# Kernel tuning notes

Hardware: AMD Instinct MI355X
Metric: run time of the kernel (lower is better)

The kernel has to match this reference:

```python
import jax, jax.numpy as jnp
import numpy as np

D = 128          # embed_d
T = 10           # MAX_NEIGHBORS
L = 2            # n_layers
B = 4096
ND, FD = 20000, 2048
NG, FG = 20000, 1024
NC, FC = 10000, 512


def setup_inputs() -> dict:
    key = jax.random.key(0)
    ks = jax.random.split(key, 18)
    inp = {
        'drug_feats': jax.random.normal(ks[0], (ND, FD), jnp.float32),
        'gene_feats': jax.random.normal(ks[1], (NG, FG), jnp.float32),
        'cell_feats': jax.random.normal(ks[2], (NC, FC), jnp.float32),
        'Wd': jax.random.normal(ks[3], (FD, D), jnp.float32) / np.sqrt(FD),
        'bd': jnp.zeros((D,), jnp.float32),
        'Wg': jax.random.normal(ks[4], (FG, D), jnp.float32) / np.sqrt(FG),
        'bg': jnp.zeros((D,), jnp.float32),
        'Wc': jax.random.normal(ks[5], (FC, D), jnp.float32) / np.sqrt(FC),
        'bc': jnp.zeros((D,), jnp.float32),
        'gru_W': jax.random.normal(ks[6], (L, 3, D, 3 * D), jnp.float32) / np.sqrt(D),
        'gru_U': jax.random.normal(ks[7], (L, 3, D, 3 * D), jnp.float32) / np.sqrt(D),
        'gru_b': jnp.zeros((L, 3, 3 * D), jnp.float32),
        'att': jax.random.normal(ks[8], (L, 2 * D), jnp.float32) / np.sqrt(2 * D),
        'ids': jax.random.randint(ks[9], (B,), 0, ND, jnp.int32),
        # neighbor ids in [-1, N-1]; -1 == PAD_VALUE
        'neigh_drug': jax.random.randint(ks[10], (B, T), 0, ND + 1, jnp.int32) - 1,
        'neigh_gene': jax.random.randint(ks[11], (B, T), 0, NG + 1, jnp.int32) - 1,
        'neigh_cell': jax.random.randint(ks[12], (B, T), 0, NC + 1, jnp.int32) - 1,
    }
    return inp


def _proj_gather(table, W, b, idx):
    # gather raw features by id (PAD -> zeros) then project, matching
    # conteng_agg + masked scatter in node_het_agg.
    mask = (idx >= 0)                              # [B, T]
    safe = jnp.clip(idx, 0, None)
    f = table[safe] @ W + b                        # [B, T, D]
    return f * mask[..., None].astype(f.dtype), mask


def _gru_seq(x, W, U, b):
    # x: [B, T, D]; torch-style GRU, returns all hidden states [B, T, D]
    xw = jnp.einsum('btd,de->bte', x, W) + b       # [B, T, 3D]
    h0 = jnp.zeros((x.shape[0], U.shape[0]), x.dtype)

    def step(h, xt):
        hu = h @ U
        xz, xr, xn = jnp.split(xt, 3, axis=-1)
        hz, hr, hn = jnp.split(hu, 3, axis=-1)
        z = jax.nn.sigmoid(xz + hz)
        r = jax.nn.sigmoid(xr + hr)
        n = jnp.tanh(xn + r * hn)
        h = (1.0 - z) * n + z * h
        return h, h

    _, hs = jax.lax.scan(step, h0, jnp.swapaxes(xw, 0, 1))
    return jnp.swapaxes(hs, 0, 1)


def reference(drug_feats, gene_feats, cell_feats, Wd, bd, Wg, bg, Wc, bc,
              gru_W, gru_U, gru_b, att, ids, neigh_drug, neigh_gene, neigh_cell):
    # self embeddings: conteng_agg(batch_ids, drug_type)
    h = drug_feats[ids] @ Wd + bd                  # [B, D]

    # neighbor content features are the layer-0 projections every layer
    # (the torch code recomputes conteng_agg per layer; result is identical)
    neigh = [
        _proj_gather(drug_feats, Wd, bd, neigh_drug),
        _proj_gather(gene_feats, Wg, bg, neigh_gene),
        _proj_gather(cell_feats, Wc, bc, neigh_cell),
    ]

    for l in range(L):
        cands = [h]
        for t, (nf, mask) in enumerate(neigh):
            out = _gru_seq(nf, gru_W[l, t], gru_U[l, t], gru_b[l, t])  # [B,T,D]
            m = mask.astype(out.dtype)
            cnt = jnp.maximum(m.sum(-1, keepdims=True), 1.0)
            cands.append((out * m[..., None]).sum(1) / cnt)            # [B,D]
        C = jnp.stack(cands, axis=1)                                   # [B,4,D]
        cat = jnp.concatenate(
            [jnp.broadcast_to(h[:, None, :], C.shape), C], axis=-1)    # [B,4,2D]
        w = jax.nn.softmax(jax.nn.leaky_relu(cat @ att[l]), axis=-1)   # [B,4]
        h = jnp.einsum('bk,bkd->bd', w, C)
    return h
```

## Files before the change

### kernel.cpp

```cpp
#include <hip/hip_runtime.h>
#include <stdint.h>


typedef short bf16x8 __attribute__((ext_vector_type(8)));
typedef float f32x4  __attribute__((ext_vector_type(4)));

__device__ __forceinline__ short f2bf(float f) {
  union { float f; unsigned u; } v; v.f = f;
  unsigned r = (v.u + 0x7fffu + ((v.u >> 16) & 1u)) >> 16;
  return (short)r;
}
__device__ __forceinline__ float b2f(short s) {
  union { float f; unsigned u; } v; v.u = ((unsigned)(unsigned short)s) << 16;
  return v.f;
}
__device__ __forceinline__ f32x4 mfma_bf16(bf16x8 a, bf16x8 b, f32x4 c) {
  return __builtin_amdgcn_mfma_f32_16x16x32_bf16(a, b, c, 0, 0, 0);
}

struct PrepW { const float* src[3]; short* dst[3]; int K[3]; };

__global__ __launch_bounds__(256) void prep_w(PrepW a) {
  const int y = blockIdx.y;
  const int K = a.K[y];
  int i = blockIdx.x * 256 + threadIdx.x;
  if (i < K * 128) {
    int k = i >> 7, n = i & 127;
    a.dst[y][(size_t)n * K + k] = f2bf(a.src[y][i]);
  }
}

__global__ __launch_bounds__(256) void prep_gru(const float* __restrict__ W,
                                                const float* __restrict__ U,
                                                short* __restrict__ dW,
                                                short* __restrict__ dU) {
  const int y = blockIdx.y;
  const float* s = (y < 6) ? W + (size_t)y * 49152 : U + (size_t)(y - 6) * 49152;
  short* d       = (y < 6) ? dW + (size_t)y * 49152 : dU + (size_t)(y - 6) * 49152;
  int i = blockIdx.x * 256 + threadIdx.x;
  if (i < 49152) {
    int k = i / 384, n = i - k * 384;
    d[(size_t)n * 128 + k] = f2bf(s[i]);
  }
}

struct ProjA {
  const float* A[3]; const short* Wt[3]; const float* bias[3];
  short* Pb[3]; float* Pf[3]; int M[3]; int K[3];
};

__global__ __launch_bounds__(256) void proj_all(ProjA p) {
  const int y = blockIdx.y;
  const int M = p.M[y];
  const int m0 = blockIdx.x * 32;
  if (m0 >= M) return;
  const int K = p.K[y];
  const float* A    = p.A[y];
  const short* Wt   = p.Wt[y];
  const float* bias = p.bias[y];
  short* Pb         = p.Pb[y];
  float* Pf         = p.Pf[y];

  __shared__ alignas(16) short As[32][136];
  __shared__ alignas(16) short Bs[128][136];
  const int tid  = threadIdx.x;
  const int lane = tid & 63;
  const int w    = tid >> 6;
  const int wc   = w * 32;
  const int quad = lane >> 4;
  const int ln   = lane & 15;

  const int arow = tid >> 3;
  const int akc  = (tid & 7) * 16;
  const int brow = tid >> 1;
  const int bkc  = (tid & 1) * 64;

  const int kIters = K >> 7;
  const int krot   = blockIdx.x % kIters;
  const int gr     = m0 + arow;
  const bool aok   = gr < M;
  const float* arp = A + (size_t)gr * K + akc;

  float4 areg[4];
  auto loadA = [&](int k0) {
    if (aok) {
      const float4* ptr = (const float4*)(arp + k0);
      areg[0] = ptr[0]; areg[1] = ptr[1]; areg[2] = ptr[2]; areg[3] = ptr[3];
    } else {
      float4 z = {0.f, 0.f, 0.f, 0.f};
      areg[0] = z; areg[1] = z; areg[2] = z; areg[3] = z;
    }
  };

  f32x4 acc[2][2];
#pragma unroll
  for (int i = 0; i < 2; i++)
#pragma unroll
    for (int j = 0; j < 2; j++) acc[i][j] = (f32x4){0.f, 0.f, 0.f, 0.f};

  loadA(krot << 7);

  for (int it = 0; it < kIters; it++) {
    int ks = krot + it; if (ks >= kIters) ks -= kIters;
    const int k0 = ks << 7;
    {
      bf16x8 v0, v1;
      v0[0]=f2bf(areg[0].x); v0[1]=f2bf(areg[0].y); v0[2]=f2bf(areg[0].z); v0[3]=f2bf(areg[0].w);
      v0[4]=f2bf(areg[1].x); v0[5]=f2bf(areg[1].y); v0[6]=f2bf(areg[1].z); v0[7]=f2bf(areg[1].w);
      v1[0]=f2bf(areg[2].x); v1[1]=f2bf(areg[2].y); v1[2]=f2bf(areg[2].z); v1[3]=f2bf(areg[2].w);
      v1[4]=f2bf(areg[3].x); v1[5]=f2bf(areg[3].y); v1[6]=f2bf(areg[3].z); v1[7]=f2bf(areg[3].w);
      *(bf16x8*)&As[arow][akc]     = v0;
      *(bf16x8*)&As[arow][akc + 8] = v1;
    }
    {
      const short* bp = Wt + (size_t)brow * K + k0 + bkc;
#pragma unroll
      for (int j = 0; j < 8; j++)
        *(bf16x8*)&Bs[brow][bkc + j * 8] = *(const bf16x8*)(bp + j * 8);
    }
    __syncthreads();
    if (it + 1 < kIters) {
      int kn = krot + it + 1; if (kn >= kIters) kn -= kIters;
      loadA(kn << 7);
    }
#pragma unroll
    for (int kt = 0; kt < 4; kt++) {
      bf16x8 af[2], bfr[2];
#pragma unroll
      for (int mi = 0; mi < 2; mi++)
        af[mi] = *(const bf16x8*)&As[mi * 16 + ln][kt * 32 + quad * 8];
#pragma unroll
      for (int nj = 0; nj < 2; nj++)
        bfr[nj] = *(const bf16x8*)&Bs[wc + nj * 16 + ln][kt * 32 + quad * 8];
#pragma unroll
      for (int mi = 0; mi < 2; mi++)
#pragma unroll
        for (int nj = 0; nj < 2; nj++)
          acc[mi][nj] = mfma_bf16(af[mi], bfr[nj], acc[mi][nj]);
    }
    __syncthreads();
  }

#pragma unroll
  for (int mi = 0; mi < 2; mi++)
#pragma unroll
    for (int nj = 0; nj < 2; nj++) {
      const int col = wc + nj * 16 + ln;
      const float bv = bias[col];
#pragma unroll
      for (int r = 0; r < 4; r++) {
        const int row = m0 + mi * 16 + quad * 4 + r;
        if (row < M) {
          const float v = acc[mi][nj][r] + bv;
          if (Pb) Pb[(size_t)row * 128 + col] = f2bf(v);
          if (Pf) Pf[(size_t)row * 128 + col] = v;
        }
      }
    }
}

__global__ __launch_bounds__(256) void gather_h0(const float* __restrict__ Pd,
                                                 const int* __restrict__ ids,
                                                 float* __restrict__ h) {
  int i = blockIdx.x * 256 + threadIdx.x;
  int b = i >> 7, d = i & 127;
  h[i] = Pd[(size_t)ids[b] * 128 + d];
}

__global__ __launch_bounds__(256) void xw_all(
    const short* __restrict__ P0, const short* __restrict__ P1,
    const short* __restrict__ P2, const int* __restrict__ n0,
    const int* __restrict__ n1, const int* __restrict__ n2,
    const short* __restrict__ gWt_all, const float* __restrict__ grub_all,
    short* __restrict__ xwT_base, int s_base) {
  const int s  = s_base + blockIdx.z;
  const int ty = s - (s / 3) * 3;
  const short* Pb  = (ty == 0) ? P0 : (ty == 1) ? P1 : P2;
  const int*   nbr = (ty == 0) ? n0 : (ty == 1) ? n1 : n2;
  const short* Wts = gWt_all + (size_t)s * 49152;
  const float* gbs = grub_all + (size_t)s * 384;
  short* xwT = xwT_base + (size_t)blockIdx.z * 40960 * 384;

  __shared__ alignas(16) short As[64][136];
  __shared__ alignas(16) short Bs[128][136];
  const int tid  = threadIdx.x;
  const int lane = tid & 63;
  const int w    = tid >> 6;
  const int wr   = (w >> 1) * 32;
  const int wc   = (w & 1) * 64;
  const int quad = lane >> 4;
  const int ln   = lane & 15;
  const int m0    = blockIdx.x * 64;
  const int nbase = blockIdx.y * 128;

  {
    const int row = tid >> 2;
    const int kc  = (tid & 3) * 32;
    const int idx = nbr[m0 + row];
    if (idx >= 0) {
      const short* p = Pb + (size_t)idx * 128 + kc;
#pragma unroll
      for (int i = 0; i < 4; i++)
        *(bf16x8*)&As[row][kc + i * 8] = *(const bf16x8*)(p + i * 8);
    } else {
      bf16x8 zv;
#pragma unroll
      for (int i = 0; i < 8; i++) zv[i] = 0;
#pragma unroll
      for (int i = 0; i < 4; i++) *(bf16x8*)&As[row][kc + i * 8] = zv;
    }
  }
  {
    const int n  = tid >> 1;
    const int kc = (tid & 1) * 64;
    const short* p = Wts + (size_t)(nbase + n) * 128 + kc;
#pragma unroll
    for (int i = 0; i < 8; i++)
      *(bf16x8*)&Bs[n][kc + i * 8] = *(const bf16x8*)(p + i * 8);
  }
  __syncthreads();

  f32x4 acc[2][4];
#pragma unroll
  for (int i = 0; i < 2; i++)
#pragma unroll
    for (int j = 0; j < 4; j++) acc[i][j] = (f32x4){0.f, 0.f, 0.f, 0.f};

#pragma unroll
  for (int kt = 0; kt < 4; kt++) {
    bf16x8 af[2], bfr[4];
#pragma unroll
    for (int mi = 0; mi < 2; mi++)
      af[mi] = *(const bf16x8*)&As[wr + mi * 16 + ln][kt * 32 + quad * 8];
#pragma unroll
    for (int nj = 0; nj < 4; nj++)
      bfr[nj] = *(const bf16x8*)&Bs[wc + nj * 16 + ln][kt * 32 + quad * 8];
#pragma unroll
    for (int mi = 0; mi < 2; mi++)
#pragma unroll
      for (int nj = 0; nj < 4; nj++)
        acc[mi][nj] = mfma_bf16(af[mi], bfr[nj], acc[mi][nj]);
  }

#pragma unroll
  for (int mi = 0; mi < 2; mi++)
#pragma unroll
    for (int nj = 0; nj < 4; nj++) {
      const int col = wc + nj * 16 + ln;
      const float bv = gbs[nbase + col];
#pragma unroll
      for (int r = 0; r < 4; r++) {
        const int rt   = m0 + wr + mi * 16 + quad * 4 + r;
        const int grow = rt / 10;
        const int st   = rt - grow * 10;
        xwT[((size_t)st * 4096 + grow) * 384 + nbase + col] =
            f2bf(acc[mi][nj][r] + bv);
      }
    }
}

__global__ __launch_bounds__(256) void scan_all(
    const short* __restrict__ xwT_base, const short* __restrict__ Ut_base,
    const int* __restrict__ n0, const int* __restrict__ n1,
    const int* __restrict__ n2, float* __restrict__ out_base, int s_base) {
  const int sz = blockIdx.y;
  const int s  = s_base + sz;
  const int ty = s - (s / 3) * 3;
  const short* xwT = xwT_base + (size_t)sz * 40960 * 384;
  const short* Utz = Ut_base + (size_t)s * 49152;
  const int*   nbr = (ty == 0) ? n0 : (ty == 1) ? n1 : n2;
  float* outp = out_base + (size_t)sz * 4096 * 128;

  __shared__ alignas(16) short hs[16][128];
  __shared__ alignas(16) short xls[16][392];
  __shared__ float mask_s[16][10];
  __shared__ float cinv[16];

  const int tid  = threadIdx.x;
  const int lane = tid & 63;
  const int w    = tid >> 6;
  const int nb   = w * 32;
  const int quad = lane >> 4;
  const int ln   = lane & 15;
  const int r0   = blockIdx.x * 16;

  if (tid < 160) {
    int i = tid / 10, tt = tid % 10;
    mask_s[i][tt] = (nbr[(r0 + i) * 10 + tt] >= 0) ? 1.f : 0.f;
  }
  {
    short* hf = &hs[0][0];
    for (int i = tid; i < 16 * 128; i += 256) hf[i] = 0;
  }
  __syncthreads();
  if (tid < 16) {
    float sm = 0.f;
    for (int tt = 0; tt < 10; tt++) sm += mask_s[tid][tt];
    cinv[tid] = 1.f / fmaxf(sm, 1.f);
  }

  bf16x8 u[3][2][4];
#pragma unroll
  for (int g = 0; g < 3; g++)
#pragma unroll
    for (int jj = 0; jj < 2; jj++)
#pragma unroll
      for (int kt = 0; kt < 4; kt++)
        u[g][jj][kt] = *(const bf16x8*)(Utz +
            (size_t)(g * 128 + nb + jj * 16 + ln) * 128 + kt * 32 + quad * 8);

  int srow[3], scol[3];
#pragma unroll
  for (int j = 0; j < 3; j++) {
    const int o = tid * 24 + j * 8;
    srow[j] = o / 384;
    scol[j] = o - srow[j] * 384;
  }

  float hreg[2][4], oacc[2][4];
#pragma unroll
  for (int jj = 0; jj < 2; jj++)
#pragma unroll
    for (int r = 0; r < 4; r++) { hreg[jj][r] = 0.f; oacc[jj][r] = 0.f; }

  __syncthreads();

  for (int st = 0; st < 10; st++) {
    bf16x8 a[4];
#pragma unroll
    for (int kt = 0; kt < 4; kt++)
      a[kt] = *(const bf16x8*)&hs[ln][kt * 32 + quad * 8];

    const short* src = xwT + ((size_t)st * 4096 + r0) * 384;
    bf16x8 xrg[3];
#pragma unroll
    for (int j = 0; j < 3; j++)
      xrg[j] = *(const bf16x8*)(src + tid * 24 + j * 8);

    f32x4 hu[3][2];
#pragma unroll
    for (int g = 0; g < 3; g++)
#pragma unroll
      for (int jj = 0; jj < 2; jj++) hu[g][jj] = (f32x4){0.f, 0.f, 0.f, 0.f};
#pragma unroll
    for (int kt = 0; kt < 4; kt++)
#pragma unroll
      for (int g = 0; g < 3; g++)
#pragma unroll
        for (int jj = 0; jj < 2; jj++)
          hu[g][jj] = mfma_bf16(a[kt], u[g][jj][kt], hu[g][jj]);

#pragma unroll
    for (int j = 0; j < 3; j++)
      *(bf16x8*)&xls[srow[j]][scol[j]] = xrg[j];
    __syncthreads();

#pragma unroll
    for (int jj = 0; jj < 2; jj++) {
      const int col = nb + jj * 16 + ln;
#pragma unroll
      for (int r = 0; r < 4; r++) {
        const int row = quad * 4 + r;
        const float xz = b2f(xls[row][col]);
        const float xr = b2f(xls[row][col + 128]);
        const float xn = b2f(xls[row][col + 256]);
        const float zg = 1.f / (1.f + __expf(-(xz + hu[0][jj][r])));
        const float rg = 1.f / (1.f + __expf(-(xr + hu[1][jj][r])));
        const float pn = xn + rg * hu[2][jj][r];
        const float e2 = __expf(2.f * pn);
        const float n  = (e2 - 1.f) / (e2 + 1.f);
        const float hn = (1.f - zg) * n + zg * hreg[jj][r];
        hreg[jj][r] = hn;
        oacc[jj][r] += hn * mask_s[row][st];
        hs[row][col] = f2bf(hn);
      }
    }
    __syncthreads();
  }

#pragma unroll
  for (int jj = 0; jj < 2; jj++)
#pragma unroll
    for (int r = 0; r < 4; r++) {
      const int row = quad * 4 + r;
      outp[(size_t)(r0 + row) * 128 + nb + jj * 16 + ln] =
          oacc[jj][r] * cinv[row];
    }
}

__global__ __launch_bounds__(256) void attn_kernel(
    const float* __restrict__ hin, const float* __restrict__ cand,
    const float* __restrict__ att, float* __restrict__ hout) {
  const int tid  = threadIdx.x;
  const int lane = tid & 63;
  const int w    = tid >> 6;
  const int gb   = blockIdx.x * 4 + w;

  const float ah0 = att[lane],       ah1 = att[lane + 64];
  const float ac0 = att[128 + lane], ac1 = att[192 + lane];

  float c0[4], c1[4];
  c0[0] = hin[(size_t)gb * 128 + lane];
  c1[0] = hin[(size_t)gb * 128 + 64 + lane];
#pragma unroll
  for (int k = 1; k < 4; k++) {
    const float* p = cand + (size_t)(k - 1) * 4096 * 128 + (size_t)gb * 128;
    c0[k] = p[lane]; c1[k] = p[64 + lane];
  }

  float sh = ah0 * c0[0] + ah1 * c1[0];
#pragma unroll
  for (int m = 1; m < 64; m <<= 1) sh += __shfl_xor(sh, m);

  float e[4];
#pragma unroll
  for (int k = 0; k < 4; k++) {
    float sv = ac0 * c0[k] + ac1 * c1[k];
#pragma unroll
    for (int m = 1; m < 64; m <<= 1) sv += __shfl_xor(sv, m);
    sv += sh;
    e[k] = (sv > 0.f) ? sv : 0.01f * sv;
  }
  const float mx = fmaxf(fmaxf(e[0], e[1]), fmaxf(e[2], e[3]));
  float wk[4], wsum = 0.f;
#pragma unroll
  for (int k = 0; k < 4; k++) { wk[k] = __expf(e[k] - mx); wsum += wk[k]; }
  const float inv = 1.f / wsum;
  float o0 = 0.f, o1 = 0.f;
#pragma unroll
  for (int k = 0; k < 4; k++) { o0 += wk[k] * c0[k]; o1 += wk[k] * c1[k]; }
  hout[(size_t)gb * 128 + lane]      = o0 * inv;
  hout[(size_t)gb * 128 + 64 + lane] = o1 * inv;
}

extern "C" void kernel_launch(void* const* d_in, const int* in_sizes, int n_in,
                              void* d_out, int out_size, void* d_ws, size_t ws_size,
                              hipStream_t stream) {
  const float* drug = (const float*)d_in[0];
  const float* gene = (const float*)d_in[1];
  const float* cell = (const float*)d_in[2];
  const float* Wd   = (const float*)d_in[3];
  const float* bd   = (const float*)d_in[4];
  const float* Wg   = (const float*)d_in[5];
  const float* bg   = (const float*)d_in[6];
  const float* Wc   = (const float*)d_in[7];
  const float* bc   = (const float*)d_in[8];
  const float* gruW = (const float*)d_in[9];
  const float* gruU = (const float*)d_in[10];
  const float* grub = (const float*)d_in[11];
  const float* att  = (const float*)d_in[12];
  const int* ids    = (const int*)d_in[13];
  const int* nbr[3] = {(const int*)d_in[14], (const int*)d_in[15],
                       (const int*)d_in[16]};

  const size_t XW_SLOT   = (size_t)40960 * 384;
  const size_t CAND_SLOT = (size_t)4096 * 128;

  const size_t need_big =
      (size_t)20000 * 128 * 4 + (size_t)20000 * 128 * 2 +
      (size_t)20000 * 128 * 2 + (size_t)10000 * 128 * 2 +
      (size_t)4096 * 128 * 4 + 6 * CAND_SLOT * 4 + 6 * XW_SLOT * 2 +
      (size_t)2048 * 128 * 2 + (size_t)1024 * 128 * 2 + (size_t)512 * 128 * 2 +
      2 * (size_t)6 * 384 * 128 * 2 + 16384 ;
  const bool big = ws_size >= need_big;

  char* ws = (char*)d_ws;
  auto alloc = [&](size_t bytes) {
    void* p = ws; ws += (bytes + 255) & ~(size_t)255; return p;
  };
  float* Pdf  = (float*)alloc((size_t)20000 * 128 * 4);
  short* Pdb  = (short*)alloc((size_t)20000 * 128 * 2);
  short* Pgb  = (short*)alloc((size_t)20000 * 128 * 2);
  short* Pcb  = (short*)alloc((size_t)10000 * 128 * 2);
  float* h    = (float*)alloc((size_t)4096 * 128 * 4);
  float* cand = (float*)alloc((big ? 6 : 3) * CAND_SLOT * 4);
  short* xwb  = (short*)alloc((big ? 6 : 1) * XW_SLOT * 2);
  short* Wdt  = (short*)alloc((size_t)2048 * 128 * 2);
  short* Wgt  = (short*)alloc((size_t)1024 * 128 * 2);
  short* Wct  = (short*)alloc((size_t)512 * 128 * 2);
  short* gWt  = (short*)alloc((size_t)6 * 384 * 128 * 2);
  short* Ut   = (short*)alloc((size_t)6 * 384 * 128 * 2);

  {
    PrepW pw;
    pw.src[0] = Wd;  pw.dst[0] = Wdt; pw.K[0] = 2048;
    pw.src[1] = Wg;  pw.dst[1] = Wgt; pw.K[1] = 1024;
    pw.src[2] = Wc;  pw.dst[2] = Wct; pw.K[2] = 512;
    prep_w<<<dim3(1024, 3), 256, 0, stream>>>(pw);
  }
  prep_gru<<<dim3(192, 12), 256, 0, stream>>>(gruW, gruU, gWt, Ut);

  {
    ProjA pa;
    pa.A[0] = drug; pa.Wt[0] = Wdt; pa.bias[0] = bd;
    pa.Pb[0] = Pdb; pa.Pf[0] = Pdf; pa.M[0] = 20000; pa.K[0] = 2048;
    pa.A[1] = gene; pa.Wt[1] = Wgt; pa.bias[1] = bg;
    pa.Pb[1] = Pgb; pa.Pf[1] = nullptr; pa.M[1] = 20000; pa.K[1] = 1024;
    pa.A[2] = cell; pa.Wt[2] = Wct; pa.bias[2] = bc;
    pa.Pb[2] = Pcb; pa.Pf[2] = nullptr; pa.M[2] = 10000; pa.K[2] = 512;
    proj_all<<<dim3(625, 3), 256, 0, stream>>>(pa);
  }
  gather_h0<<<2048, 256, 0, stream>>>(Pdf, ids, h);

  if (big) {
    xw_all<<<dim3(640, 3, 6), 256, 0, stream>>>(
        Pdb, Pgb, Pcb, nbr[0], nbr[1], nbr[2], gWt, grub, xwb, 0);
    scan_all<<<dim3(256, 6), 256, 0, stream>>>(
        xwb, Ut, nbr[0], nbr[1], nbr[2], cand, 0);
    attn_kernel<<<1024, 256, 0, stream>>>(h, cand, att, h);
    attn_kernel<<<1024, 256, 0, stream>>>(
        h, cand + 3 * CAND_SLOT, att + 256, (float*)d_out);
  } else {
    for (int l = 0; l < 2; l++) {
      for (int t = 0; t < 3; t++) {
        const int s = l * 3 + t;
        xw_all<<<dim3(640, 3, 1), 256, 0, stream>>>(
            Pdb, Pgb, Pcb, nbr[0], nbr[1], nbr[2], gWt, grub, xwb, s);
        scan_all<<<dim3(256, 1), 256, 0, stream>>>(
            xwb, Ut, nbr[0], nbr[1], nbr[2], cand + (size_t)t * CAND_SLOT, s);
      }
      attn_kernel<<<1024, 256, 0, stream>>>(
          h, cand, att + l * 256, (l == 1) ? (float*)d_out : h);
    }
  }
}
```

Measured before the change: 543.3 us.

## Double-buffer A tile and load B fragments directly from global in projection GEMM

```diff
diff --git a/kernel.cpp b/kernel.cpp
--- a/kernel.cpp
+++ b/kernel.cpp
@@ -49,7 +49,7 @@
   short* Pb[3]; float* Pf[3]; int M[3]; int K[3];
 };
 
-__global__ __launch_bounds__(256) void proj_all(ProjA p) {
+__global__ __launch_bounds__(256, 5) void proj_all(ProjA p) {
   const int y = blockIdx.y;
   const int M = p.M[y];
   const int m0 = blockIdx.x * 32;
@@ -61,25 +61,25 @@
   short* Pb         = p.Pb[y];
   float* Pf         = p.Pf[y];
 
-  __shared__ alignas(16) short As[32][136];
-  __shared__ alignas(16) short Bs[128][136];
+  __shared__ alignas(16) short As[2][32][136];
   const int tid  = threadIdx.x;
   const int lane = tid & 63;
   const int w    = tid >> 6;
   const int wc   = w * 32;
   const int quad = lane >> 4;
   const int ln   = lane & 15;
+  const int kq   = quad * 8;
 
   const int arow = tid >> 3;
   const int akc  = (tid & 7) * 16;
-  const int brow = tid >> 1;
-  const int bkc  = (tid & 1) * 64;
 
   const int kIters = K >> 7;
   const int krot   = blockIdx.x % kIters;
   const int gr     = m0 + arow;
   const bool aok   = gr < M;
   const float* arp = A + (size_t)gr * K + akc;
+  const short* brp0 = Wt + (size_t)(wc + ln) * K + kq;
+  const short* brp1 = Wt + (size_t)(wc + 16 + ln) * K + kq;
 
   float4 areg[4];
   auto loadA = [&](int k0) {
@@ -91,6 +91,15 @@
       areg[0] = z; areg[1] = z; areg[2] = z; areg[3] = z;
     }
   };
+  auto cvtStore = [&](int buf) {
+    bf16x8 v0, v1;
+    v0[0]=f2bf(areg[0].x); v0[1]=f2bf(areg[0].y); v0[2]=f2bf(areg[0].z); v0[3]=f2bf(areg[0].w);
+    v0[4]=f2bf(areg[1].x); v0[5]=f2bf(areg[1].y); v0[6]=f2bf(areg[1].z); v0[7]=f2bf(areg[1].w);
+    v1[0]=f2bf(areg[2].x); v1[1]=f2bf(areg[2].y); v1[2]=f2bf(areg[2].z); v1[3]=f2bf(areg[2].w);
+    v1[4]=f2bf(areg[3].x); v1[5]=f2bf(areg[3].y); v1[6]=f2bf(areg[3].z); v1[7]=f2bf(areg[3].w);
+    *(bf16x8*)&As[buf][arow][akc]     = v0;
+    *(bf16x8*)&As[buf][arow][akc + 8] = v1;
+  };
 
   f32x4 acc[2][2];
 #pragma unroll
@@ -99,45 +108,33 @@
     for (int j = 0; j < 2; j++) acc[i][j] = (f32x4){0.f, 0.f, 0.f, 0.f};
 
   loadA(krot << 7);
+  cvtStore(0);
+  __syncthreads();
 
   for (int it = 0; it < kIters; it++) {
     int ks = krot + it; if (ks >= kIters) ks -= kIters;
     const int k0 = ks << 7;
-    {
-      bf16x8 v0, v1;
-      v0[0]=f2bf(areg[0].x); v0[1]=f2bf(areg[0].y); v0[2]=f2bf(areg[0].z); v0[3]=f2bf(areg[0].w);
-      v0[4]=f2bf(areg[1].x); v0[5]=f2bf(areg[1].y); v0[6]=f2bf(areg[1].z); v0[7]=f2bf(areg[1].w);
-      v1[0]=f2bf(areg[2].x); v1[1]=f2bf(areg[2].y); v1[2]=f2bf(areg[2].z); v1[3]=f2bf(areg[2].w);
-      v1[4]=f2bf(areg[3].x); v1[5]=f2bf(areg[3].y); v1[6]=f2bf(areg[3].z); v1[7]=f2bf(areg[3].w);
-      *(bf16x8*)&As[arow][akc]     = v0;
-      *(bf16x8*)&As[arow][akc + 8] = v1;
-    }
-    {
-      const short* bp = Wt + (size_t)brow * K + k0 + bkc;
-#pragma unroll
-      for (int j = 0; j < 8; j++)
-        *(bf16x8*)&Bs[brow][bkc + j * 8] = *(const bf16x8*)(bp + j * 8);
-    }
-    __syncthreads();
     if (it + 1 < kIters) {
-      int kn = krot + it + 1; if (kn >= kIters) kn -= kIters;
+      int kn = ks + 1; if (kn >= kIters) kn -= kIters;
       loadA(kn << 7);
     }
+    bf16x8 bfr[2][4];
 #pragma unroll
     for (int kt = 0; kt < 4; kt++) {
-      bf16x8 af[2], bfr[2];
-#pragma unroll
-      for (int mi = 0; mi < 2; mi++)
-        af[mi] = *(const bf16x8*)&As[mi * 16 + ln][kt * 32 + quad * 8];
-#pragma unroll
-      for (int nj = 0; nj < 2; nj++)
-        bfr[nj] = *(const bf16x8*)&Bs[wc + nj * 16 + ln][kt * 32 + quad * 8];
-#pragma unroll
-      for (int mi = 0; mi < 2; mi++)
-#pragma unroll
-        for (int nj = 0; nj < 2; nj++)
-          acc[mi][nj] = mfma_bf16(af[mi], bfr[nj], acc[mi][nj]);
-    }
+      bfr[0][kt] = *(const bf16x8*)(brp0 + k0 + kt * 32);
+      bfr[1][kt] = *(const bf16x8*)(brp1 + k0 + kt * 32);
+    }
+    const int buf = it & 1;
+#pragma unroll
+    for (int kt = 0; kt < 4; kt++) {
+      bf16x8 af0 = *(const bf16x8*)&As[buf][ln][kt * 32 + kq];
+      bf16x8 af1 = *(const bf16x8*)&As[buf][16 + ln][kt * 32 + kq];
+      acc[0][0] = mfma_bf16(af0, bfr[0][kt], acc[0][0]);
+      acc[0][1] = mfma_bf16(af0, bfr[1][kt], acc[0][1]);
+      acc[1][0] = mfma_bf16(af1, bfr[0][kt], acc[1][0]);
+      acc[1][1] = mfma_bf16(af1, bfr[1][kt], acc[1][1]);
+    }
+    if (it + 1 < kIters) cvtStore(buf ^ 1);
     __syncthreads();
   }
 
```

After: 549.7 us. About the same (+1.2%).
